# Kernel tuning notes

Measured on AMD Instinct MI355X. Metric: run time of the kernel, lower is better.

## Reference

```python
import jax, jax.numpy as jnp
import numpy as np

EMBED = 1024
HEAD_COUNT = 16
HEAD_DIM = EMBED // HEAD_COUNT  # 64


def setup_inputs() -> dict:
    key = jax.random.key(0)
    ks = jax.random.split(key, 5)
    N, S = 2, 1024
    keys_ = jax.random.normal(ks[0], (N, S, EMBED), dtype=jnp.float32)
    query = jax.random.normal(ks[1], (N, S, EMBED), dtype=jnp.float32)
    values = jax.random.normal(ks[2], (N, S, EMBED), dtype=jnp.float32)
    mask = jnp.ones((N, 1, S, S), dtype=jnp.int32)
    W_out = jax.random.normal(ks[3], (EMBED, EMBED), dtype=jnp.float32) * (1.0 / np.sqrt(EMBED))
    b_out = jax.random.normal(ks[4], (EMBED,), dtype=jnp.float32) * 0.01
    return {"keys": keys_, "query": query, "values": values, "mask": mask,
            "W_out": W_out, "b_out": b_out}


def reference(keys, query, values, mask, W_out, b_out):
    N, Sq, E = query.shape
    Sk = keys.shape[1]
    Sv = values.shape[1]
    # Faithful to the original: reshape to (N, L, head_dimensions, head_count);
    # einsum 'nqhd,nkhd->nhqk' uses h = head_dimensions (64) as the head axis.
    q = query.reshape(N, Sq, HEAD_DIM, HEAD_COUNT)
    k = keys.reshape(N, Sk, HEAD_DIM, HEAD_COUNT)
    v = values.reshape(N, Sv, HEAD_DIM, HEAD_COUNT)
    ene = jnp.einsum('nqhd,nkhd->nhqk', q, k)  # [N, 64, Sq, Sk]
    ene = jnp.where(mask == 0, jnp.float32(-1e20), ene)
    attn = jax.nn.softmax(ene / jnp.sqrt(jnp.float32(E)), axis=3)
    out = jnp.einsum('nhql,nlhd->nqhd', attn, v).reshape(N, Sq, EMBED)
    # forward_out Linear (with bias): y = x @ W.T + b
    return out @ W_out.T + b_out
```

## Files before the change

kernel.cpp:

```cpp
#include <hip/hip_runtime.h>
#include <hip/hip_bf16.h>


#define S_LEN 1024
#define EMB   1024
#define HD    16

typedef __attribute__((ext_vector_type(8)))  short short8;
typedef __attribute__((ext_vector_type(16))) float floatx16;

#if __has_builtin(__builtin_amdgcn_exp2f)
#define EXP2(x) __builtin_amdgcn_exp2f(x)
#else
#define EXP2(x) exp2f(x)
#endif

union PkU { __hip_bfloat162 h; unsigned int u; };
__device__ __forceinline__ unsigned int pk2(float a, float b) {
    PkU p; p.h = __float22bfloat162_rn(make_float2(a, b)); return p.u;
}
union Frag { unsigned int u[4]; short8 s; };

__device__ __forceinline__ void async16(const void* g, void* l) {
    __builtin_amdgcn_global_load_lds(
        (const __attribute__((address_space(1))) unsigned int*)g,
        (__attribute__((address_space(3))) unsigned int*)l, 16, 0, 0);
}

__global__ __launch_bounds__(256) void attn_kernel(
    const float* __restrict__ keys,
    const float* __restrict__ query,
    const float* __restrict__ values,
    const float* __restrict__ W,
    unsigned short* __restrict__ Xt,
    unsigned short* __restrict__ Wt)
{
    const int b   = blockIdx.x;
    const int hn  = b & 127;
    const int q0  = (b >> 7) * 128;
    const int h   = hn & 63;
    const int n   = hn >> 6;
    const int tid = threadIdx.x;
    const int w   = tid >> 6;
    const int l   = tid & 63;
    const int l31 = l & 31;
    const int hi  = l >> 5;

    __shared__ unsigned short KL[2][2048];
    __shared__ unsigned short VL[2][4096];

    #pragma unroll
    for (int bq = 0; bq < 2; ++bq)
        for (int i = tid; i < 4096; i += 256)
            VL[bq][i] = (((i >> 3) & 31) == 16) ? (unsigned short)0x3F80
                                                : (unsigned short)0;

    const int q = q0 + 32 * w + l31;
    Frag qf;
    {
        const float* qp = &query[(size_t)(n * S_LEN + q) * EMB + h * HD + 8 * hi];
        float4 a  = *(const float4*)qp;
        float4 b4 = *(const float4*)(qp + 4);
        const float sc = 0.04508422009f;
        qf.u[0] = pk2(a.x * sc, a.y * sc);
        qf.u[1] = pk2(a.z * sc, a.w * sc);
        qf.u[2] = pk2(b4.x * sc, b4.y * sc);
        qf.u[3] = pk2(b4.z * sc, b4.w * sc);
    }

    floatx16 O;
    #pragma unroll
    for (int i = 0; i < 16; ++i) O[i] = 0.0f;
    floatx16 fz;
    #pragma unroll
    for (int i = 0; i < 16; ++i) fz[i] = 0.0f;

    float4 kreg[2];
    float  vreg[2][4];

    auto LOAD = [&](int kt) {
        #pragma unroll
        for (int p = 0; p < 2; ++p) {
            int idx = tid + 256 * p;
            int key = idx >> 2, part = idx & 3;
            kreg[p] = *(const float4*)&keys[
                (size_t)(n * S_LEN + kt * 128 + key) * EMB + h * HD + 4 * part];
        }
        #pragma unroll
        for (int p = 0; p < 2; ++p) {
            int idx = tid + 256 * p;
            int vd = idx & 15, g4 = idx >> 4;
            int s = g4 >> 2, hi2 = (g4 >> 1) & 1, jh = g4 & 1;
            int key0 = kt * 128 + s * 16 + 4 * hi2 + 8 * jh;
            const float* vp = &values[(size_t)(n * S_LEN + key0) * EMB + h * HD + vd];
            vreg[p][0] = vp[0];
            vreg[p][1] = vp[EMB];
            vreg[p][2] = vp[2 * EMB];
            vreg[p][3] = vp[3 * EMB];
        }
    };
    auto WRITE = [&](int bq) {
        #pragma unroll
        for (int p = 0; p < 2; ++p) {
            int idx = tid + 256 * p;
            int key = idx >> 2, part = idx & 3;
            int kidx = (key >> 5) * 512 + ((key & 31) + 32 * (part >> 1)) * 8
                     + (part & 1) * 4;
            *(uint2*)&KL[bq][kidx] =
                make_uint2(pk2(kreg[p].x, kreg[p].y), pk2(kreg[p].z, kreg[p].w));
        }
        #pragma unroll
        for (int p = 0; p < 2; ++p) {
            int idx = tid + 256 * p;
            int vd = idx & 15, g4 = idx >> 4;
            int s = g4 >> 2, hi2 = (g4 >> 1) & 1, jh = g4 & 1;
            int dst = s * 512 + (vd + 32 * hi2) * 8 + 4 * jh;
            *(uint2*)&VL[bq][dst] =
                make_uint2(pk2(vreg[p][0], vreg[p][1]), pk2(vreg[p][2], vreg[p][3]));
        }
    };

    LOAD(0);
    WRITE(0);
    __syncthreads();

    for (int kt = 0; kt < 8; ++kt) {
        const int cur = kt & 1;
        if (kt < 7) LOAD(kt + 1);
        const unsigned short* KLb = KL[cur];
        const unsigned short* VLb = VL[cur];
        #pragma unroll
        for (int t = 0; t < 4; ++t) {
            Frag kf;
            kf.s = *(const short8*)&KLb[t * 512 + l * 8];
            floatx16 S = __builtin_amdgcn_mfma_f32_32x32x16_bf16(kf.s, qf.s, fz, 0, 0, 0);
            #pragma unroll
            for (int u = 0; u < 2; ++u) {
                float e0 = EXP2(S[8 * u + 0]), e1 = EXP2(S[8 * u + 1]);
                float e2 = EXP2(S[8 * u + 2]), e3 = EXP2(S[8 * u + 3]);
                float e4 = EXP2(S[8 * u + 4]), e5 = EXP2(S[8 * u + 5]);
                float e6 = EXP2(S[8 * u + 6]), e7 = EXP2(S[8 * u + 7]);
                Frag pf;
                pf.u[0] = pk2(e0, e1); pf.u[1] = pk2(e2, e3);
                pf.u[2] = pk2(e4, e5); pf.u[3] = pk2(e6, e7);
                Frag vf;
                vf.s = *(const short8*)&VLb[(2 * t + u) * 512 + l * 8];
                O = __builtin_amdgcn_mfma_f32_32x32x16_bf16(vf.s, pf.s, O, 0, 0, 0);
            }
        }
        if (kt < 7) WRITE(cur ^ 1);
        __syncthreads();
    }

    float d  = O[8];
    float dd = __shfl_xor(d, 32, 64);
    float inv = 1.0f / (hi ? dd : d);

    const int m   = n * S_LEN + q;
    const int rb  = (m >> 5) & 1;
    const int r31 = m & 31;
    size_t off0 = ((size_t)(m >> 6) * 16 + (h >> 2)) * 4096
                + (size_t)(rb * 4 + (h & 3)) * 512 + r31 * 8 + 4 * hi;
    uint2 g0 = make_uint2(pk2(O[0] * inv, O[1] * inv), pk2(O[2] * inv, O[3] * inv));
    uint2 g1 = make_uint2(pk2(O[4] * inv, O[5] * inv), pk2(O[6] * inv, O[7] * inv));
    *(uint2*)&Xt[off0]       = g0;
    *(uint2*)&Xt[off0 + 256] = g1;

    {
        const int gid = b * 256 + tid;
        const int e  = gid >> 8;
        const int k  = (gid & 255) * 4;
        float4 wv = *(const float4*)&W[(size_t)e * 1024 + k];
        const int nt  = e >> 6, row = e & 63;
        const int kt  = k >> 6, c   = k & 63;
        const int seg = c >> 3,  c7 = c & 7;
        size_t dst = (size_t)(nt * 16 + kt) * 4096
                   + (size_t)((row >> 5) * 4 + (seg >> 1)) * 512
                   + ((row & 31) + 32 * (seg & 1)) * 8 + c7;
        *(uint2*)&Wt[dst] = make_uint2(pk2(wv.x, wv.y), pk2(wv.z, wv.w));
    }
}

__global__ __launch_bounds__(256) void proj_kernel(
    const unsigned short* __restrict__ Xt,
    const unsigned short* __restrict__ Wt,
    const float* __restrict__ bias,
    float* __restrict__ Y)
{
    __shared__ unsigned short AL[2][4096];
    __shared__ unsigned short BL[2][4096];

    const int tid = threadIdx.x;
    const int w   = tid >> 6;
    const int l   = tid & 63;
    const int l31 = l & 31;
    const int hi  = l >> 5;
    const int mt    = blockIdx.y;
    const int ntile = blockIdx.x;
    const int r  = w & 1;
    const int ct = w >> 1;

    const unsigned short* Xbase = Xt + (size_t)mt    * 16 * 4096;
    const unsigned short* Wbase = Wt + (size_t)ntile * 16 * 4096;

    floatx16 acc;
    #pragma unroll
    for (int i = 0; i < 16; ++i) acc[i] = 0.0f;

    auto stage = [&](unsigned short* dst, const unsigned short* src) {
        #pragma unroll
        for (int p = 0; p < 2; ++p) {
            int c = w * 2 + p;
            async16(src + (size_t)(c * 64 + l) * 8, dst + (c * 64 + l) * 8);
        }
    };

    stage(AL[0], Xbase);
    stage(BL[0], Wbase);
    __syncthreads();

    for (int k = 0; k < 16; ++k) {
        const int cur = k & 1;
        if (k < 15) {
            stage(AL[cur ^ 1], Xbase + (size_t)(k + 1) * 4096);
            stage(BL[cur ^ 1], Wbase + (size_t)(k + 1) * 4096);
        }
        #pragma unroll
        for (int s = 0; s < 4; ++s) {
            Frag af, bf;
            af.s = *(const short8*)&AL[cur][(r  * 4 + s) * 512 + l * 8];
            bf.s = *(const short8*)&BL[cur][(ct * 4 + s) * 512 + l * 8];
            acc = __builtin_amdgcn_mfma_f32_32x32x16_bf16(af.s, bf.s, acc, 0, 0, 0);
        }
        __syncthreads();
    }

    const int e = ntile * 64 + 32 * ct + l31;
    const float bv = bias[e];
    #pragma unroll
    for (int reg = 0; reg < 16; ++reg) {
        int m = mt * 64 + 32 * r + (reg & 3) + 8 * (reg >> 2) + 4 * hi;
        Y[(size_t)m * 1024 + e] = acc[reg] + bv;
    }
}

extern "C" void kernel_launch(void* const* d_in, const int* in_sizes, int n_in,
                              void* d_out, int out_size, void* d_ws, size_t ws_size,
                              hipStream_t stream) {
    const float* keys   = (const float*)d_in[0];
    const float* query  = (const float*)d_in[1];
    const float* values = (const float*)d_in[2];
    const float* W_out  = (const float*)d_in[4];
    const float* b_out  = (const float*)d_in[5];
    float* Y = (float*)d_out;

    unsigned short* Xt = (unsigned short*)d_ws;
    unsigned short* Wt = (unsigned short*)d_ws + (size_t)2 * 1024 * 1024;

    attn_kernel<<<1024, 256, 0, stream>>>(keys, query, values, W_out, Xt, Wt);
    proj_kernel<<<dim3(16, 32), 256, 0, stream>>>(Xt, Wt, b_out, Y);
}
```

Measured before the change: 125.0 us.

## Deepen projection GEMM pipeline to four LDS buffers with prefetch distance two

The output projection kernel now keeps four LDS stages and issues async global-to-LDS loads two k-tiles ahead. Manual vmcnt waits and a single raw barrier per iteration replace the double-buffer scheme and its two __syncthreads. This is meant to hide more global-load latency and cut barrier overhead. It doubles LDS use per block, which may lower occupancy, and relies on exact vmcnt accounting for correctness.

```diff
diff --git a/kernel.cpp b/kernel.cpp
--- a/kernel.cpp
+++ b/kernel.cpp
@@ -187,8 +187,8 @@
     const float* __restrict__ bias,
     float* __restrict__ Y)
 {
-    __shared__ unsigned short AL[2][4096];
-    __shared__ unsigned short BL[2][4096];
+    __shared__ unsigned short AL[4][4096];
+    __shared__ unsigned short BL[4][4096];
 
     const int tid = threadIdx.x;
     const int w   = tid >> 6;
@@ -207,32 +207,45 @@
     #pragma unroll
     for (int i = 0; i < 16; ++i) acc[i] = 0.0f;
 
-    auto stage = [&](unsigned short* dst, const unsigned short* src) {
+    auto stage = [&](int buf, int k) {
+        const unsigned short* sA = Xbase + (size_t)k * 4096;
+        const unsigned short* sB = Wbase + (size_t)k * 4096;
         #pragma unroll
         for (int p = 0; p < 2; ++p) {
             int c = w * 2 + p;
-            async16(src + (size_t)(c * 64 + l) * 8, dst + (c * 64 + l) * 8);
+            async16(sA + (c * 64 + l) * 8, &AL[buf][(c * 64 + l) * 8]);
+        }
+        #pragma unroll
+        for (int p = 0; p < 2; ++p) {
+            int c = w * 2 + p;
+            async16(sB + (c * 64 + l) * 8, &BL[buf][(c * 64 + l) * 8]);
         }
     };
 
-    stage(AL[0], Xbase);
-    stage(BL[0], Wbase);
-    __syncthreads();
+    stage(0, 0);
+    stage(1, 1);
 
     for (int k = 0; k < 16; ++k) {
-        const int cur = k & 1;
-        if (k < 15) {
-            stage(AL[cur ^ 1], Xbase + (size_t)(k + 1) * 4096);
-            stage(BL[cur ^ 1], Wbase + (size_t)(k + 1) * 4096);
-        }
+        if (k < 14) {
+            stage((k + 2) & 3, k + 2);
+            asm volatile("s_waitcnt vmcnt(8)" ::: "memory");
+        } else if (k == 14) {
+            asm volatile("s_waitcnt vmcnt(4)" ::: "memory");
+        } else {
+            asm volatile("s_waitcnt vmcnt(0)" ::: "memory");
+        }
+        __builtin_amdgcn_s_barrier();
+        __builtin_amdgcn_sched_barrier(0);
+
+        const unsigned short* Ab = AL[k & 3];
+        const unsigned short* Bb = BL[k & 3];
         #pragma unroll
         for (int s = 0; s < 4; ++s) {
             Frag af, bf;
-            af.s = *(const short8*)&AL[cur][(r  * 4 + s) * 512 + l * 8];
-            bf.s = *(const short8*)&BL[cur][(ct * 4 + s) * 512 + l * 8];
+            af.s = *(const short8*)&Ab[(r  * 4 + s) * 512 + l * 8];
+            bf.s = *(const short8*)&Bb[(ct * 4 + s) * 512 + l * 8];
             acc = __builtin_amdgcn_mfma_f32_32x32x16_bf16(af.s, bf.s, acc, 0, 0, 0);
         }
-        __syncthreads();
     }
 
     const int e = ntile * 64 + 32 * ct + l31;
```

After: 120.5 us. 1.04x faster.
